# Optimization experiments

Measured on AMD Instinct MI355X. Metric: run time of the kernel, lower is better.

Reference implementation:

```python
import jax, jax.numpy as jnp
import numpy as np

N_EDGE = 1_000_000
N_NODE = 100_000
EDGE_DIM = 64
N_RADIAL = 16
UP_DIM = 256


def silu(x):
    return x * jax.nn.sigmoid(x)  # Swish(beta=1.0)


def setup_inputs() -> dict:
    key = jax.random.key(0)
    ks = jax.random.split(key, 12)
    s = 0.05
    return {
        "x": jax.random.normal(ks[0], (N_EDGE, EDGE_DIM), jnp.float32),
        "rbf": jax.random.normal(ks[1], (N_EDGE, N_RADIAL), jnp.float32),
        "idx_i": jax.random.randint(ks[2], (N_EDGE,), 0, N_NODE, jnp.int32).astype(jnp.int64),
        "num_nodes": N_NODE,
        "W_rbf": jax.random.normal(ks[3], (N_RADIAL, EDGE_DIM), jnp.float32) * s,
        "W_up": jax.random.normal(ks[4], (EDGE_DIM, UP_DIM), jnp.float32) * s,
        "W1": jax.random.normal(ks[5], (UP_DIM, UP_DIM), jnp.float32) * s,
        "b1": jnp.zeros((UP_DIM,), jnp.float32),
        "W2": jax.random.normal(ks[6], (UP_DIM, UP_DIM), jnp.float32) * s,
        "b2": jnp.zeros((UP_DIM,), jnp.float32),
        "W3": jax.random.normal(ks[7], (UP_DIM, UP_DIM), jnp.float32) * s,
        "b3": jnp.zeros((UP_DIM,), jnp.float32),
        "W_out": jax.random.normal(ks[8], (UP_DIM, 1), jnp.float32) * s,
    }


def reference(x, rbf, idx_i, num_nodes, W_rbf, W_up, W1, b1, W2, b2, W3, b3, W_out):
    # Gate edge embeddings by rbf projection, scatter-add to center nodes.
    e = (rbf @ W_rbf) * x                              # (n_edge, edge_dim)
    h = jax.ops.segment_sum(e, idx_i, num_segments=num_nodes)  # (n_node, edge_dim)
    h = h @ W_up                                       # (n_node, up_dim)
    h = silu(h @ W1 + b1)
    h = silu(h @ W2 + b2)
    h = silu(h @ W3 + b3)
    return h @ W_out                                   # (n_node, out_dim)
```

## Files before the change

kernel.cpp:

```cpp
#include <hip/hip_runtime.h>
#include <hip/hip_bf16.h>

#define EDGE_DIM 64
#define UPD 256

typedef __attribute__((ext_vector_type(8))) short bf16x8;
typedef __attribute__((ext_vector_type(4))) float f32x4;

__device__ __forceinline__ short f2bf(float v) {
    __hip_bfloat16 b = __float2bfloat16(v);
    return *(short*)&b;
}
__device__ __forceinline__ float bf2f(short s) {
    __hip_bfloat16 b = *(__hip_bfloat16*)&s;
    return __bfloat162float(b);
}

__device__ __forceinline__ void split_trunc(float v, short& hi, short& lo) {
    unsigned u = __float_as_uint(v);
    unsigned hu = u & 0xFFFF0000u;
    hi = (short)(hu >> 16);
    float rem = v - __uint_as_float(hu);
    lo = (short)(__float_as_uint(rem) >> 16);
}

__global__ __launch_bounds__(256) void zero_ws_kernel(
    float4* __restrict__ h4, long long n4, int* __restrict__ count, int nn) {
    const long long t = (long long)blockIdx.x * blockDim.x + threadIdx.x;
    const long long stride = (long long)gridDim.x * blockDim.x;
    const float4 z = {0.f, 0.f, 0.f, 0.f};
    for (long long i = t; i < n4; i += stride) h4[i] = z;
    for (long long i = t; i < nn; i += stride) count[i] = 0;
}

__device__ __forceinline__ int detect_use64_block(const void* idx_v,
                                                  int n_edge, int nn,
                                                  int* bad_s) {
    if (threadIdx.x == 0) *bad_s = 0;
    __syncthreads();
    const long long* p = (const long long*)idx_v;
    int i = threadIdx.x;
    if (i < 256 && i < n_edge) {
        long long v = p[i];
        if (v < 0 || v >= (long long)nn) *bad_s = 1;
    }
    __syncthreads();
    return !(*bad_s);
}

__global__ __launch_bounds__(256) void count_kernel(
    const void* __restrict__ idx_v, int n_edge, int nn,
    int* __restrict__ count) {
    __shared__ int bad_s;
    const int use64 = detect_use64_block(idx_v, n_edge, nn, &bad_s);
    const long long* i64 = (const long long*)idx_v;
    const int* i32 = (const int*)idx_v;
    for (int e = blockIdx.x * blockDim.x + threadIdx.x; e < n_edge;
         e += gridDim.x * blockDim.x) {
        int n = use64 ? (int)i64[e] : i32[e];
        atomicAdd(&count[n], 1);
    }
}

__global__ __launch_bounds__(256) void scan_a(const int* __restrict__ count,
                                              int* __restrict__ base,
                                              int* __restrict__ partial,
                                              int nn) {
    __shared__ int s[256];
    const int tid = threadIdx.x;
    const int i0 = blockIdx.x * 1024 + tid * 4;
    int c[4], tsum = 0;
#pragma unroll
    for (int j = 0; j < 4; ++j) {
        c[j] = (i0 + j < nn) ? count[i0 + j] : 0;
        tsum += c[j];
    }
    s[tid] = tsum;
    __syncthreads();
    for (int off = 1; off < 256; off <<= 1) {
        int v = (tid >= off) ? s[tid - off] : 0;
        __syncthreads();
        s[tid] += v;
        __syncthreads();
    }
    int run = s[tid] - tsum;
    if (tid == 255) partial[blockIdx.x] = s[255];
#pragma unroll
    for (int j = 0; j < 4; ++j) {
        if (i0 + j < nn) base[i0 + j] = run;
        run += c[j];
    }
}

__global__ __launch_bounds__(256) void scan_b(int* __restrict__ partial,
                                              int nblk) {
    __shared__ int s[256];
    const int tid = threadIdx.x;
    int v = (tid < nblk) ? partial[tid] : 0;
    s[tid] = v;
    __syncthreads();
    for (int off = 1; off < 256; off <<= 1) {
        int u = (tid >= off) ? s[tid - off] : 0;
        __syncthreads();
        s[tid] += u;
        __syncthreads();
    }
    if (tid < nblk) partial[tid] = s[tid] - v;
}

__global__ __launch_bounds__(256) void scan_c(int* __restrict__ base,
                                              int* __restrict__ cursor,
                                              const int* __restrict__ partial,
                                              int nn, int n_edge) {
    const int tid = threadIdx.x;
    const int b = blockIdx.x;
    const int add = partial[b];
    const int i0 = b * 1024 + tid * 4;
#pragma unroll
    for (int j = 0; j < 4; ++j) {
        int i = i0 + j;
        if (i < nn) {
            int v = base[i] + add;
            base[i] = v;
            cursor[i] = v;
        }
    }
    if (b == 0 && tid == 0) base[nn] = n_edge;
}

__global__ __launch_bounds__(256) void fill_order_kernel(
    const void* __restrict__ idx_v, int n_edge, int nn,
    int* __restrict__ cursor, int* __restrict__ order,
    int* __restrict__ nodeof) {
    __shared__ int bad_s;
    const int use64 = detect_use64_block(idx_v, n_edge, nn, &bad_s);
    const long long* i64 = (const long long*)idx_v;
    const int* i32 = (const int*)idx_v;
    for (int e = blockIdx.x * blockDim.x + threadIdx.x; e < n_edge;
         e += gridDim.x * blockDim.x) {
        int n = use64 ? (int)i64[e] : i32[e];
        int p = atomicAdd(&cursor[n], 1);
        order[p] = e;
        nodeof[p] = n;
    }
}

__global__ __launch_bounds__(256) void segsum2_kernel(
    const float* __restrict__ x, const float* __restrict__ rbf,
    const int* __restrict__ order, const int* __restrict__ nodeof,
    const float* __restrict__ Wrbf, float* __restrict__ h, int n_edge) {
    const int lane = threadIdx.x & 63;
    float wreg[16];
#pragma unroll
    for (int q = 0; q < 16; ++q) wreg[q] = Wrbf[q * EDGE_DIM + lane];

    const int wid = threadIdx.x >> 6;
    const int nchunks = (n_edge + 63) >> 6;
    const int stride = gridDim.x * 4;

    for (int c = blockIdx.x * 4 + wid; c < nchunks; c += stride) {
        const int s0 = c * 64;
        int slot = s0 + lane;
        if (slot >= n_edge) slot = n_edge - 1;
        const int ev = order[slot];
        const int ndv = nodeof[slot];

        float acc = 0.f;
        int cur = -1;
#pragma unroll
        for (int g = 0; g < 4; ++g) {
            const int j0 = g * 16;
            int e[16];
            float xv[16], rv[16];
#pragma unroll
            for (int j = 0; j < 16; ++j) {
                e[j] = __builtin_amdgcn_readlane(ev, j0 + j);
                xv[j] = x[(size_t)e[j] * EDGE_DIM + lane];
                rv[j] = rbf[(size_t)e[j] * 16 + (lane & 15)];
            }
#pragma unroll
            for (int j = 0; j < 16; ++j) {
                float gate = 0.f;
#pragma unroll
                for (int q = 0; q < 16; ++q) {
                    int rb = __builtin_amdgcn_readlane(
                        __float_as_int(rv[j]), q);
                    gate = fmaf(__int_as_float(rb), wreg[q], gate);
                }
                const int nd = __builtin_amdgcn_readlane(ndv, j0 + j);
                if (s0 + j0 + j < n_edge) {
                    if (nd != cur) {
                        if (cur >= 0)
                            atomicAdd(&h[(size_t)cur * EDGE_DIM + lane], acc);
                        cur = nd;
                        acc = 0.f;
                    }
                    acc = fmaf(gate, xv[j], acc);
                }
            }
        }
        if (cur >= 0) atomicAdd(&h[(size_t)cur * EDGE_DIM + lane], acc);
    }
}

__device__ __forceinline__ void pack_body(const float* __restrict__ W,
                                          short* __restrict__ out, int t) {
    int l = t & 63, f = t >> 6;
    int kt = f >> 4, nt = f & 15;
    int kbase = kt * 32 + (l >> 4) * 8;
    int col = nt * 16 + (l & 15);
#pragma unroll
    for (int j = 0; j < 8; ++j) {
        float v = W[(kbase + j) * UPD + col];
        short hb = f2bf(v);
        short lb = f2bf(v - bf2f(hb));
        out[f * 1024 + l * 8 + j] = hb;
        out[f * 1024 + 512 + l * 8 + j] = lb;
    }
}

__global__ __launch_bounds__(256) void pack_all_kernel(
    const float* __restrict__ Wup, const float* __restrict__ W1,
    const float* __restrict__ W2, const float* __restrict__ W3,
    short* __restrict__ oup, short* __restrict__ o1, short* __restrict__ o2,
    short* __restrict__ o3) {
    const int b = blockIdx.x;
    if (b < 8) {
        pack_body(Wup, oup, b * 256 + threadIdx.x);
    } else if (b < 40) {
        pack_body(W1, o1, (b - 8) * 256 + threadIdx.x);
    } else if (b < 72) {
        pack_body(W2, o2, (b - 40) * 256 + threadIdx.x);
    } else {
        pack_body(W3, o3, (b - 72) * 256 + threadIdx.x);
    }
}

template <int NK>
__device__ __forceinline__ void mm_layer(const short* AH, const short* AL,
                                         const short* __restrict__ Wpk,
                                         int lr, int lh, int lane, int wq,
                                         f32x4 acc[4][4]) {
    bf16x8 bc[4][2];
#pragma unroll
    for (int nf = 0; nf < 4; ++nf) {
        const short* p = Wpk + (wq * 4 + nf) * 1024 + lane * 8;
        bc[nf][0] = *(const bf16x8*)(p);
        bc[nf][1] = *(const bf16x8*)(p + 512);
    }
#pragma unroll
    for (int kt = 0; kt < NK; ++kt) {
        bf16x8 a[4][2];
#pragma unroll
        for (int m = 0; m < 4; ++m) {
            int r = m * 16 + lr;
            int ch = (kt * 4 + lh) ^ (r & 7);
            int off = r * 256 + ch * 8;
            a[m][0] = *(const bf16x8*)(AH + off);
            a[m][1] = *(const bf16x8*)(AL + off);
        }
        bf16x8 bn[4][2];
        if (kt + 1 < NK) {
#pragma unroll
            for (int nf = 0; nf < 4; ++nf) {
                const short* p =
                    Wpk + ((kt + 1) * 16 + wq * 4 + nf) * 1024 + lane * 8;
                bn[nf][0] = *(const bf16x8*)(p);
                bn[nf][1] = *(const bf16x8*)(p + 512);
            }
        }
#pragma unroll
        for (int m = 0; m < 4; ++m)
#pragma unroll
            for (int nf = 0; nf < 4; ++nf)
                acc[m][nf] = __builtin_amdgcn_mfma_f32_16x16x32_bf16(
                    a[m][0], bc[nf][0], acc[m][nf], 0, 0, 0);
#pragma unroll
        for (int m = 0; m < 4; ++m)
#pragma unroll
            for (int nf = 0; nf < 4; ++nf)
                acc[m][nf] = __builtin_amdgcn_mfma_f32_16x16x32_bf16(
                    a[m][0], bc[nf][1], acc[m][nf], 0, 0, 0);
#pragma unroll
        for (int m = 0; m < 4; ++m)
#pragma unroll
            for (int nf = 0; nf < 4; ++nf)
                acc[m][nf] = __builtin_amdgcn_mfma_f32_16x16x32_bf16(
                    a[m][1], bc[nf][0], acc[m][nf], 0, 0, 0);
        if (kt + 1 < NK) {
#pragma unroll
            for (int nf = 0; nf < 4; ++nf) {
                bc[nf][0] = bn[nf][0];
                bc[nf][1] = bn[nf][1];
            }
        }
    }
}

template <bool ACT>
__device__ __forceinline__ void epilogue_store(f32x4 acc[4][4], short* AH,
                                               short* AL,
                                               const float* __restrict__ bias,
                                               int lr, int lh, int wq) {
    float bv[4] = {0.f, 0.f, 0.f, 0.f};
    if (bias) {
#pragma unroll
        for (int nf = 0; nf < 4; ++nf) bv[nf] = bias[wq * 64 + nf * 16 + lr];
    }
#pragma unroll
    for (int m = 0; m < 4; ++m)
#pragma unroll
        for (int nf = 0; nf < 4; ++nf) {
            int c = wq * 64 + nf * 16 + lr;
#pragma unroll
            for (int reg = 0; reg < 4; ++reg) {
                float v = acc[m][nf][reg] + bv[nf];
                if (ACT) {
                    float e = __expf(-v);
                    v = v * __builtin_amdgcn_rcpf(1.f + e);
                }
                int r = m * 16 + lh * 4 + reg;
                short hb, lb;
                split_trunc(v, hb, lb);
                int off = r * 256 + (((c >> 3) ^ (r & 7)) * 8) + (c & 7);
                AH[off] = hb;
                AL[off] = lb;
            }
        }
}

__global__ __launch_bounds__(256, 2) void node_mlp_mfma(
    const float* __restrict__ h,
    const short* __restrict__ Wup_pk, const short* __restrict__ W1_pk,
    const short* __restrict__ W2_pk, const short* __restrict__ W3_pk,
    const float* __restrict__ b1, const float* __restrict__ b2,
    const float* __restrict__ b3, const float* __restrict__ W_out,
    float* __restrict__ out, int nn) {
    __shared__ short AH[64 * 256];
    __shared__ short AL[64 * 256];
    __shared__ float Bpart[64 * 4];

    const int tid = threadIdx.x;
    const int lane = tid & 63, wq = tid >> 6;
    const int lr = lane & 15, lh = lane >> 4;
    const int node0 = blockIdx.x * 64;

#pragma unroll
    for (int i = 0; i < 4; ++i) {
        int idx4 = tid + i * 256;
        int r = idx4 >> 4, c4 = idx4 & 15;
        float4 v = {0.f, 0.f, 0.f, 0.f};
        if (node0 + r < nn)
            v = *(const float4*)(h + (size_t)(node0 + r) * EDGE_DIM + c4 * 4);
        short h0, h1, h2, h3, l0, l1, l2, l3;
        split_trunc(v.x, h0, l0);
        split_trunc(v.y, h1, l1);
        split_trunc(v.z, h2, l2);
        split_trunc(v.w, h3, l3);
        int off = r * 256 + (((c4 >> 1) ^ (r & 7)) * 8) + (c4 & 1) * 4;
        uint2 hw, lw;
        hw.x = (unsigned short)h0 | ((unsigned)(unsigned short)h1 << 16);
        hw.y = (unsigned short)h2 | ((unsigned)(unsigned short)h3 << 16);
        lw.x = (unsigned short)l0 | ((unsigned)(unsigned short)l1 << 16);
        lw.y = (unsigned short)l2 | ((unsigned)(unsigned short)l3 << 16);
        *(uint2*)(AH + off) = hw;
        *(uint2*)(AL + off) = lw;
    }
    __syncthreads();

    f32x4 acc[4][4];

#pragma unroll
    for (int m = 0; m < 4; ++m)
#pragma unroll
        for (int n = 0; n < 4; ++n) acc[m][n] = (f32x4){0.f, 0.f, 0.f, 0.f};
    mm_layer<2>(AH, AL, Wup_pk, lr, lh, lane, wq, acc);
    __syncthreads();
    epilogue_store<false>(acc, AH, AL, nullptr, lr, lh, wq);
    __syncthreads();

#pragma unroll
    for (int m = 0; m < 4; ++m)
#pragma unroll
        for (int n = 0; n < 4; ++n) acc[m][n] = (f32x4){0.f, 0.f, 0.f, 0.f};
    mm_layer<8>(AH, AL, W1_pk, lr, lh, lane, wq, acc);
    __syncthreads();
    epilogue_store<true>(acc, AH, AL, b1, lr, lh, wq);
    __syncthreads();

#pragma unroll
    for (int m = 0; m < 4; ++m)
#pragma unroll
        for (int n = 0; n < 4; ++n) acc[m][n] = (f32x4){0.f, 0.f, 0.f, 0.f};
    mm_layer<8>(AH, AL, W2_pk, lr, lh, lane, wq, acc);
    __syncthreads();
    epilogue_store<true>(acc, AH, AL, b2, lr, lh, wq);
    __syncthreads();

#pragma unroll
    for (int m = 0; m < 4; ++m)
#pragma unroll
        for (int n = 0; n < 4; ++n) acc[m][n] = (f32x4){0.f, 0.f, 0.f, 0.f};
    mm_layer<8>(AH, AL, W3_pk, lr, lh, lane, wq, acc);

    float b3v[4], wo[4];
#pragma unroll
    for (int nf = 0; nf < 4; ++nf) {
        int c = wq * 64 + nf * 16 + lr;
        b3v[nf] = b3[c];
        wo[nf] = W_out[c];
    }
#pragma unroll
    for (int m = 0; m < 4; ++m) {
#pragma unroll
        for (int reg = 0; reg < 4; ++reg) {
            float s = 0.f;
#pragma unroll
            for (int nf = 0; nf < 4; ++nf) {
                float v = acc[m][nf][reg] + b3v[nf];
                float e = __expf(-v);
                v = v * __builtin_amdgcn_rcpf(1.f + e);
                s = fmaf(v, wo[nf], s);
            }
            s += __shfl_xor(s, 1);
            s += __shfl_xor(s, 2);
            s += __shfl_xor(s, 4);
            s += __shfl_xor(s, 8);
            if (lr == 0) Bpart[(m * 16 + lh * 4 + reg) * 4 + wq] = s;
        }
    }
    __syncthreads();
    if (tid < 64) {
        float s = Bpart[tid * 4] + Bpart[tid * 4 + 1] + Bpart[tid * 4 + 2] +
                  Bpart[tid * 4 + 3];
        if (node0 + tid < nn) out[node0 + tid] = s;
    }
}

extern "C" void kernel_launch(void* const* d_in, const int* in_sizes, int n_in,
                              void* d_out, int out_size, void* d_ws, size_t ws_size,
                              hipStream_t stream) {
    const float* x     = (const float*)d_in[0];
    const float* rbf   = (const float*)d_in[1];
    const void*  idx   = d_in[2];
    const float* W_rbf = (const float*)d_in[4];
    const float* W_up  = (const float*)d_in[5];
    const float* W1    = (const float*)d_in[6];
    const float* b1    = (const float*)d_in[7];
    const float* W2    = (const float*)d_in[8];
    const float* b2    = (const float*)d_in[9];
    const float* W3    = (const float*)d_in[10];
    const float* b3    = (const float*)d_in[11];
    const float* W_out = (const float*)d_in[12];
    float* out = (float*)d_out;

    const int n_edge = in_sizes[0] / EDGE_DIM;
    const int nn = out_size;

    char* p = (char*)d_ws;
    float* h = (float*)p;            p += (size_t)nn * EDGE_DIM * sizeof(float);
    short* wup_pk = (short*)p;       p += 32 * 1024 * sizeof(short);
    short* w1_pk = (short*)p;        p += 128 * 1024 * sizeof(short);
    short* w2_pk = (short*)p;        p += 128 * 1024 * sizeof(short);
    short* w3_pk = (short*)p;        p += 128 * 1024 * sizeof(short);
    int* count = (int*)p;            p += (size_t)nn * sizeof(int);
    int* base = (int*)p;             p += (size_t)(nn + 1) * sizeof(int);
    int* cursor = (int*)p;           p += (size_t)nn * sizeof(int);
    int* partial = (int*)p;          p += 1024;
    int* order = (int*)p;            p += (size_t)n_edge * sizeof(int);
    int* nodeof = (int*)p;

    const int nblk_scan = (nn + 1023) / 1024;

    zero_ws_kernel<<<2048, 256, 0, stream>>>(
        (float4*)h, (long long)nn * EDGE_DIM / 4, count, nn);
    pack_all_kernel<<<104, 256, 0, stream>>>(W_up, W1, W2, W3, wup_pk, w1_pk,
                                             w2_pk, w3_pk);
    count_kernel<<<2048, 256, 0, stream>>>(idx, n_edge, nn, count);
    scan_a<<<nblk_scan, 256, 0, stream>>>(count, base, partial, nn);
    scan_b<<<1, 256, 0, stream>>>(partial, nblk_scan);
    scan_c<<<nblk_scan, 256, 0, stream>>>(base, cursor, partial, nn, n_edge);
    fill_order_kernel<<<2048, 256, 0, stream>>>(idx, n_edge, nn, cursor,
                                                order, nodeof);
    const int nchunks = (n_edge + 63) / 64;
    const int nblk_seg = (nchunks + 3) / 4;
    segsum2_kernel<<<nblk_seg, 256, 0, stream>>>(x, rbf, order, nodeof,
                                                 W_rbf, h, n_edge);

    const int nb = (nn + 63) / 64;
    node_mlp_mfma<<<nb, 256, 0, stream>>>(h, wup_pk, w1_pk, w2_pk, w3_pk,
                                          b1, b2, b3, W_out, out, nn);
}
```

Baseline: 352.9 us.

## Vectorize index loads, pack order/node pairs, double-buffer segment-sum gathers

The count and fill kernels now read four indices per thread with vector loads. The fill kernel writes edge id and node id as one int2 instead of two separate arrays. The segment-sum kernel issues the gathers for the next 16-edge group before consuming the current one, using two register buffers, so memory latency overlaps with the gate FMAs. This raises register pressure, which may reduce occupancy, and workspace alignment is padded to keep the int2 array aligned.

```diff
diff --git a/kernel.cpp b/kernel.cpp
--- a/kernel.cpp
+++ b/kernel.cpp
@@ -53,12 +53,33 @@
     int* __restrict__ count) {
     __shared__ int bad_s;
     const int use64 = detect_use64_block(idx_v, n_edge, nn, &bad_s);
-    const long long* i64 = (const long long*)idx_v;
-    const int* i32 = (const int*)idx_v;
-    for (int e = blockIdx.x * blockDim.x + threadIdx.x; e < n_edge;
-         e += gridDim.x * blockDim.x) {
-        int n = use64 ? (int)i64[e] : i32[e];
-        atomicAdd(&count[n], 1);
+    const int t = blockIdx.x * blockDim.x + threadIdx.x;
+    const int nt = gridDim.x * blockDim.x;
+    const int n4 = n_edge >> 2;
+    if (use64) {
+        const longlong2* p2 = (const longlong2*)idx_v;
+        for (int i = t; i < n4; i += nt) {
+            longlong2 a = p2[i * 2], b = p2[i * 2 + 1];
+            atomicAdd(&count[(int)a.x], 1);
+            atomicAdd(&count[(int)a.y], 1);
+            atomicAdd(&count[(int)b.x], 1);
+            atomicAdd(&count[(int)b.y], 1);
+        }
+        const long long* p = (const long long*)idx_v;
+        for (int e = n4 * 4 + t; e < n_edge; e += nt)
+            atomicAdd(&count[(int)p[e]], 1);
+    } else {
+        const int4* p4 = (const int4*)idx_v;
+        for (int i = t; i < n4; i += nt) {
+            int4 v = p4[i];
+            atomicAdd(&count[v.x], 1);
+            atomicAdd(&count[v.y], 1);
+            atomicAdd(&count[v.z], 1);
+            atomicAdd(&count[v.w], 1);
+        }
+        const int* p = (const int*)idx_v;
+        for (int e = n4 * 4 + t; e < n_edge; e += nt)
+            atomicAdd(&count[p[e]], 1);
     }
 }
 
@@ -130,25 +151,87 @@
 
 __global__ __launch_bounds__(256) void fill_order_kernel(
     const void* __restrict__ idx_v, int n_edge, int nn,
-    int* __restrict__ cursor, int* __restrict__ order,
-    int* __restrict__ nodeof) {
+    int* __restrict__ cursor, int2* __restrict__ ordnode) {
     __shared__ int bad_s;
     const int use64 = detect_use64_block(idx_v, n_edge, nn, &bad_s);
-    const long long* i64 = (const long long*)idx_v;
-    const int* i32 = (const int*)idx_v;
-    for (int e = blockIdx.x * blockDim.x + threadIdx.x; e < n_edge;
-         e += gridDim.x * blockDim.x) {
-        int n = use64 ? (int)i64[e] : i32[e];
-        int p = atomicAdd(&cursor[n], 1);
-        order[p] = e;
-        nodeof[p] = n;
-    }
-}
-
-__global__ __launch_bounds__(256) void segsum2_kernel(
+    const int t = blockIdx.x * blockDim.x + threadIdx.x;
+    const int nt = gridDim.x * blockDim.x;
+    const int n4 = n_edge >> 2;
+    if (use64) {
+        const longlong2* p2 = (const longlong2*)idx_v;
+        for (int i = t; i < n4; i += nt) {
+            longlong2 a = p2[i * 2], b = p2[i * 2 + 1];
+            int e0 = i * 4;
+            int nd;
+            nd = (int)a.x;
+            ordnode[atomicAdd(&cursor[nd], 1)] = make_int2(e0 + 0, nd);
+            nd = (int)a.y;
+            ordnode[atomicAdd(&cursor[nd], 1)] = make_int2(e0 + 1, nd);
+            nd = (int)b.x;
+            ordnode[atomicAdd(&cursor[nd], 1)] = make_int2(e0 + 2, nd);
+            nd = (int)b.y;
+            ordnode[atomicAdd(&cursor[nd], 1)] = make_int2(e0 + 3, nd);
+        }
+        const long long* p = (const long long*)idx_v;
+        for (int e = n4 * 4 + t; e < n_edge; e += nt) {
+            int nd = (int)p[e];
+            ordnode[atomicAdd(&cursor[nd], 1)] = make_int2(e, nd);
+        }
+    } else {
+        const int4* p4 = (const int4*)idx_v;
+        for (int i = t; i < n4; i += nt) {
+            int4 v = p4[i];
+            int e0 = i * 4;
+            ordnode[atomicAdd(&cursor[v.x], 1)] = make_int2(e0 + 0, v.x);
+            ordnode[atomicAdd(&cursor[v.y], 1)] = make_int2(e0 + 1, v.y);
+            ordnode[atomicAdd(&cursor[v.z], 1)] = make_int2(e0 + 2, v.z);
+            ordnode[atomicAdd(&cursor[v.w], 1)] = make_int2(e0 + 3, v.w);
+        }
+        const int* p = (const int*)idx_v;
+        for (int e = n4 * 4 + t; e < n_edge; e += nt) {
+            int nd = p[e];
+            ordnode[atomicAdd(&cursor[nd], 1)] = make_int2(e, nd);
+        }
+    }
+}
+
+#define SEG_ISSUE(G, E, XV, RV)                                      \
+    {                                                                \
+        const int j0_ = (G) * 16;                                    \
+        _Pragma("unroll") for (int j = 0; j < 16; ++j) {             \
+            E[j] = __builtin_amdgcn_readlane(ev, j0_ + j);           \
+            XV[j] = x[(size_t)E[j] * EDGE_DIM + lane];               \
+            RV[j] = rbf[(size_t)E[j] * 16 + (lane & 15)];            \
+        }                                                            \
+    }
+
+#define SEG_CONSUME(G, XV, RV)                                       \
+    {                                                                \
+        const int j0_ = (G) * 16;                                    \
+        _Pragma("unroll") for (int j = 0; j < 16; ++j) {             \
+            float gate = 0.f;                                        \
+            _Pragma("unroll") for (int q = 0; q < 16; ++q) {         \
+                int rb =                                             \
+                    __builtin_amdgcn_readlane(__float_as_int(RV[j]), q); \
+                gate = fmaf(__int_as_float(rb), wreg[q], gate);      \
+            }                                                        \
+            const int nd = __builtin_amdgcn_readlane(ndv, j0_ + j);  \
+            if (s0 + j0_ + j < n_edge) {                             \
+                if (nd != cur) {                                     \
+                    if (cur >= 0)                                    \
+                        atomicAdd(&h[(size_t)cur * EDGE_DIM + lane], acc); \
+                    cur = nd;                                        \
+                    acc = 0.f;                                       \
+                }                                                    \
+                acc = fmaf(gate, XV[j], acc);                        \
+            }                                                        \
+        }                                                            \
+    }
+
+__global__ __launch_bounds__(256) void segsum3_kernel(
     const float* __restrict__ x, const float* __restrict__ rbf,
-    const int* __restrict__ order, const int* __restrict__ nodeof,
-    const float* __restrict__ Wrbf, float* __restrict__ h, int n_edge) {
+    const int2* __restrict__ ordnode, const float* __restrict__ Wrbf,
+    float* __restrict__ h, int n_edge) {
     const int lane = threadIdx.x & 63;
     float wreg[16];
 #pragma unroll
@@ -162,43 +245,24 @@
         const int s0 = c * 64;
         int slot = s0 + lane;
         if (slot >= n_edge) slot = n_edge - 1;
-        const int ev = order[slot];
-        const int ndv = nodeof[slot];
+        const int2 on = ordnode[slot];
+        const int ev = on.x;
+        const int ndv = on.y;
 
         float acc = 0.f;
         int cur = -1;
-#pragma unroll
-        for (int g = 0; g < 4; ++g) {
-            const int j0 = g * 16;
-            int e[16];
-            float xv[16], rv[16];
-#pragma unroll
-            for (int j = 0; j < 16; ++j) {
-                e[j] = __builtin_amdgcn_readlane(ev, j0 + j);
-                xv[j] = x[(size_t)e[j] * EDGE_DIM + lane];
-                rv[j] = rbf[(size_t)e[j] * 16 + (lane & 15)];
-            }
-#pragma unroll
-            for (int j = 0; j < 16; ++j) {
-                float gate = 0.f;
-#pragma unroll
-                for (int q = 0; q < 16; ++q) {
-                    int rb = __builtin_amdgcn_readlane(
-                        __float_as_int(rv[j]), q);
-                    gate = fmaf(__int_as_float(rb), wreg[q], gate);
-                }
-                const int nd = __builtin_amdgcn_readlane(ndv, j0 + j);
-                if (s0 + j0 + j < n_edge) {
-                    if (nd != cur) {
-                        if (cur >= 0)
-                            atomicAdd(&h[(size_t)cur * EDGE_DIM + lane], acc);
-                        cur = nd;
-                        acc = 0.f;
-                    }
-                    acc = fmaf(gate, xv[j], acc);
-                }
-            }
-        }
+        int eA[16], eB[16];
+        float xvA[16], xvB[16], rvA[16], rvB[16];
+
+        SEG_ISSUE(0, eA, xvA, rvA);
+        SEG_ISSUE(1, eB, xvB, rvB);
+        SEG_CONSUME(0, xvA, rvA);
+        SEG_ISSUE(2, eA, xvA, rvA);
+        SEG_CONSUME(1, xvB, rvB);
+        SEG_ISSUE(3, eB, xvB, rvB);
+        SEG_CONSUME(2, xvA, rvA);
+        SEG_CONSUME(3, xvB, rvB);
+
         if (cur >= 0) atomicAdd(&h[(size_t)cur * EDGE_DIM + lane], acc);
     }
 }
@@ -464,11 +528,10 @@
     short* w2_pk = (short*)p;        p += 128 * 1024 * sizeof(short);
     short* w3_pk = (short*)p;        p += 128 * 1024 * sizeof(short);
     int* count = (int*)p;            p += (size_t)nn * sizeof(int);
-    int* base = (int*)p;             p += (size_t)(nn + 1) * sizeof(int);
+    int* base = (int*)p;             p += (size_t)(nn + 1) * sizeof(int) + 12;
     int* cursor = (int*)p;           p += (size_t)nn * sizeof(int);
     int* partial = (int*)p;          p += 1024;
-    int* order = (int*)p;            p += (size_t)n_edge * sizeof(int);
-    int* nodeof = (int*)p;
+    int2* ordnode = (int2*)p;
 
     const int nblk_scan = (nn + 1023) / 1024;
 
@@ -481,11 +544,11 @@
     scan_b<<<1, 256, 0, stream>>>(partial, nblk_scan);
     scan_c<<<nblk_scan, 256, 0, stream>>>(base, cursor, partial, nn, n_edge);
     fill_order_kernel<<<2048, 256, 0, stream>>>(idx, n_edge, nn, cursor,
-                                                order, nodeof);
+                                                ordnode);
     const int nchunks = (n_edge + 63) / 64;
     const int nblk_seg = (nchunks + 3) / 4;
-    segsum2_kernel<<<nblk_seg, 256, 0, stream>>>(x, rbf, order, nodeof,
-                                                 W_rbf, h, n_edge);
+    segsum3_kernel<<<nblk_seg, 256, 0, stream>>>(x, rbf, ordnode, W_rbf, h,
+                                                 n_edge);
 
     const int nb = (nn + 63) / 64;
     node_mlp_mfma<<<nb, 256, 0, stream>>>(h, wup_pk, w1_pk, w2_pk, w3_pk,
```

Result: no change. 354.3 us (+0.4%).
